# Kernel optimization log

Measured on AMD Instinct MI355X. Metric: run time of the kernel, lower is better.

## Reference

```python
import jax, jax.numpy as jnp
import numpy as np

B, SX, SY, D = 64, 512, 512, 1024


def setup_inputs() -> dict:
    key = jax.random.key(0)
    k1, k2, k3, k4 = jax.random.split(key, 4)
    x = jax.random.normal(k1, (B, SX, D), dtype=jnp.float32)
    y = jax.random.normal(k2, (B, SY, D), dtype=jnp.float32)
    # Keras 'uniform' init ~ U(-0.05, 0.05); scale kept small and realistic
    W = jax.random.uniform(k3, (D, D), dtype=jnp.float32, minval=-0.05, maxval=0.05)
    b = jax.random.uniform(k4, (D,), dtype=jnp.float32, minval=-0.05, maxval=0.05)
    return {"x": x, "y": y, "W": W, "b": b}


def reference(x, y, W, b):
    # proj: (x @ W + b) -> [B, Sx, D]
    proj = jnp.einsum('bsd,de->bse', x, W) + b
    # attention scores: proj @ y^T -> [B, Sx, Sy]
    att = jnp.einsum('bsd,btd->bst', proj, y)
    # row-wise stable softmax over last axis (matches manual max-subtract softmax)
    nor = jax.nn.softmax(att, axis=-1)
    # weighted sum over y -> [B, Sx, D]
    return jnp.einsum('bst,btd->bsd', nor, y)
```

## Files before the change

### kernel.cpp

```cpp
#include <hip/hip_runtime.h>


typedef float  f32x4  __attribute__((ext_vector_type(4)));
typedef _Float16 f16x8 __attribute__((ext_vector_type(8)));
typedef _Float16 f16x4 __attribute__((ext_vector_type(4)));
typedef __bf16 bf16x8 __attribute__((ext_vector_type(8)));
typedef __bf16 bf16x4 __attribute__((ext_vector_type(4)));

#define MFMA_F16(a, b, c)  __builtin_amdgcn_mfma_f32_16x16x32_f16((a), (b), (c), 0, 0, 0)
#define MFMA_BF16(a, b, c) __builtin_amdgcn_mfma_f32_16x16x32_bf16((a), (b), (c), 0, 0, 0)

__device__ __forceinline__ void async16(const void* g, void* lds) {
    __builtin_amdgcn_global_load_lds(
        (const __attribute__((address_space(1))) unsigned int*)g,
        (__attribute__((address_space(3))) unsigned int*)lds, 16, 0, 0);
}


__global__ void prep_y_kernel(const float* __restrict__ y, _Float16* __restrict__ yf,
                              _Float16* __restrict__ yT)
{
    __shared__ _Float16 LT[64][72];
    const int tid = threadIdx.x;
    const int b   = blockIdx.x >> 7;
    const int rem = blockIdx.x & 127;
    const int sy0 = (rem >> 4) * 64;
    const int d0  = (rem & 15) * 64;
    const int r0 = tid >> 4;
    const int c4 = (tid & 15) * 4;
    #pragma unroll
    for (int i = 0; i < 4; ++i) {
        const int r = r0 + i * 16;
        const float4 v = *(const float4*)&y[((size_t)b * 512 + sy0 + r) * 1024 + d0 + c4];
        const f16x4 hv = {(_Float16)v.x, (_Float16)v.y, (_Float16)v.z, (_Float16)v.w};
        *(f16x4*)&yf[((size_t)b * 512 + sy0 + r) * 1024 + d0 + c4] = hv;
        #pragma unroll
        for (int cc = 0; cc < 4; ++cc) {
            const int c = (cc + (tid & 3)) & 3;
            LT[c4 + c][r] = hv[c];
        }
    }
    __syncthreads();
    #pragma unroll
    for (int i = 0; i < 4; ++i) {
        const int dr = r0 + i * 16;
        const f16x4 v = *(const f16x4*)&LT[dr][(tid & 15) * 4];
        *(f16x4*)&yT[((size_t)b * 1024 + d0 + dr) * 512 + sy0 + (tid & 15) * 4] = v;
    }
}

__global__ void cvt_hl_kernel(const float4* __restrict__ in, f16x4* __restrict__ oh,
                              f16x4* __restrict__ ol, int n4)
{
    int i = blockIdx.x * blockDim.x + threadIdx.x;
    const int stride = gridDim.x * blockDim.x;
    for (; i < n4; i += stride) {
        const float4 v = in[i];
        const _Float16 h0 = (_Float16)v.x, h1 = (_Float16)v.y,
                       h2 = (_Float16)v.z, h3 = (_Float16)v.w;
        oh[i] = (f16x4){h0, h1, h2, h3};
        ol[i] = (f16x4){(_Float16)(v.x - (float)h0), (_Float16)(v.y - (float)h1),
                        (_Float16)(v.z - (float)h2), (_Float16)(v.w - (float)h3)};
    }
}

__global__ __launch_bounds__(256, 3)
void proj_f16_kernel(const _Float16* __restrict__ xh, const _Float16* __restrict__ xl,
                     const float* __restrict__ W, const float* __restrict__ bias,
                     char* __restrict__ outc)
{
    __shared__ _Float16 Xh[128][32];
    __shared__ _Float16 Xl[128][32];
    __shared__ _Float16 Wf[128][32];

    const int tid = threadIdx.x, lane = tid & 63, wave = tid >> 6;
    const int swz = (blockIdx.x & 7) * 256 + (blockIdx.x >> 3);
    const int m0 = (swz >> 3) * 128, n0 = (swz & 7) * 128;
    const int wm = (wave >> 1) * 64, wn = (wave & 1) * 64;
    const int ar = lane & 15;
    const int qs  = ((lane >> 4) ^ ((lane >> 1) & 3)) * 8;
    const int gcS = ((lane & 3) ^ ((lane >> 3) & 3)) * 8;

    f32x4 acc[4][4];
    #pragma unroll
    for (int i = 0; i < 4; ++i)
        #pragma unroll
        for (int j = 0; j < 4; ++j)
            acc[i][j] = (f32x4){0.f, 0.f, 0.f, 0.f};

    const int lrow = lane >> 2;
    const int wkb = tid & 7;
    const int wqn = tid >> 3;
    const int wn4 = wqn * 4;

    for (int k0 = 0; k0 < 1024; k0 += 32) {
        __syncthreads();
        #pragma unroll
        for (int t = 0; t < 2; ++t) {
            const int r = wave * 32 + t * 16 + lrow;
            async16(&xh[(size_t)(m0 + r) * 1024 + k0 + gcS], &Xh[wave * 32 + t * 16][0]);
            async16(&xl[(size_t)(m0 + r) * 1024 + k0 + gcS], &Xl[wave * 32 + t * 16][0]);
        }
        {
            const size_t wb = (size_t)(k0 + wkb * 4) * 1024 + n0 + wn4;
            const float4 v0 = *(const float4*)&W[wb];
            const float4 v1 = *(const float4*)&W[wb + 1024];
            const float4 v2 = *(const float4*)&W[wb + 2048];
            const float4 v3 = *(const float4*)&W[wb + 3072];
            const float rv[4][4] = {{v0.x, v0.y, v0.z, v0.w},
                                    {v1.x, v1.y, v1.z, v1.w},
                                    {v2.x, v2.y, v2.z, v2.w},
                                    {v3.x, v3.y, v3.z, v3.w}};
            #pragma unroll
            for (int j = 0; j < 4; ++j) {
                const int R = wn4 + j;
                const f16x4 hv = {(_Float16)rv[0][j], (_Float16)rv[1][j],
                                  (_Float16)rv[2][j], (_Float16)rv[3][j]};
                const int c = (wkb >> 1) ^ ((R >> 1) & 3);
                *(f16x4*)&Wf[R][c * 8 + (wkb & 1) * 4] = hv;
            }
        }
        __syncthreads();

        f16x8 ah[4], al[4], bf[4];
        #pragma unroll
        for (int f = 0; f < 4; ++f) {
            ah[f] = *(const f16x8*)&Xh[wm + f * 16 + ar][qs];
            al[f] = *(const f16x8*)&Xl[wm + f * 16 + ar][qs];
            bf[f] = *(const f16x8*)&Wf[wn + f * 16 + ar][qs];
        }
        #pragma unroll
        for (int i = 0; i < 4; ++i)
            #pragma unroll
            for (int j = 0; j < 4; ++j) {
                acc[i][j] = MFMA_F16(ah[i], bf[j], acc[i][j]);
                acc[i][j] = MFMA_F16(al[i], bf[j], acc[i][j]);
            }
    }

    const int q4 = (lane >> 4) * 4;
    #pragma unroll
    for (int j = 0; j < 4; ++j) {
        const int n = n0 + wn + j * 16 + ar;
        const float bv = bias[n];
        #pragma unroll
        for (int i = 0; i < 4; ++i)
            #pragma unroll
            for (int r = 0; r < 4; ++r) {
                const int R = m0 + wm + i * 16 + q4 + r;
                const float v = acc[i][j][r] + bv;
                const _Float16 h = (_Float16)v;
                const _Float16 l = (_Float16)(v - (float)h);
                _Float16* rowp = (_Float16*)(outc + (size_t)R * 4096);
                rowp[n] = h;
                rowp[1024 + n] = l;
            }
    }
}

__global__ __launch_bounds__(256, 2)
void attn_f16_kernel(const _Float16* __restrict__ yf, const _Float16* __restrict__ yT,
                     char* __restrict__ outc)
{
    __shared__ __align__(16) char smem[74752];
    _Float16 (*Yst)[32]   = (_Float16(*)[32])smem;
    _Float16 (*Pbuf)[520] = (_Float16(*)[520])smem;
    _Float16 (*Yt)[32]    = (_Float16(*)[32])(smem + 66560);

    const int tid = threadIdx.x, lane = tid & 63, wave = tid >> 6;
    const int swz = (blockIdx.x & 7) * 64 + (blockIdx.x >> 3);
    const int b = swz >> 3, sx0 = (swz & 7) * 64;
    const int pbase = b * 512 + sx0;
    const int ar = lane & 15, q = lane >> 4, qk = q * 8;
    const int qs  = (q ^ ((lane >> 1) & 3)) * 8;
    const int gcS = ((lane & 3) ^ ((lane >> 3) & 3)) * 8;
    const int lrow = lane >> 2;
    const size_t ybase = (size_t)b * 512 * 1024;

    f32x4 s[32];
    #pragma unroll
    for (int t = 0; t < 32; ++t) s[t] = (f32x4){0.f, 0.f, 0.f, 0.f};

    const _Float16* prow = (const _Float16*)(outc + (size_t)(pbase + wave * 16 + ar) * 4096);

    for (int k0 = 0; k0 < 1024; k0 += 32) {
        __syncthreads();
        #pragma unroll
        for (int t = 0; t < 8; ++t) {
            const int r = wave * 128 + t * 16 + lrow;
            async16(&yf[ybase + (size_t)r * 1024 + k0 + gcS], &Yst[wave * 128 + t * 16][0]);
        }
        const f16x8 a_h = *(const f16x8*)(prow + k0 + qk);
        const f16x8 a_l = *(const f16x8*)(prow + 1024 + k0 + qk);
        __syncthreads();
        #pragma unroll
        for (int t = 0; t < 32; ++t) {
            const f16x8 bfrag = *(const f16x8*)&Yst[t * 16 + ar][qs];
            s[t] = MFMA_F16(a_h, bfrag, s[t]);
            s[t] = MFMA_F16(a_l, bfrag, s[t]);
        }
    }

    #pragma unroll
    for (int r = 0; r < 4; ++r) {
        float m = -3.0e38f;
        #pragma unroll
        for (int t = 0; t < 32; ++t) m = fmaxf(m, s[t][r]);
        #pragma unroll
        for (int off = 1; off < 16; off <<= 1) m = fmaxf(m, __shfl_xor(m, off, 64));
        float sum = 0.f;
        #pragma unroll
        for (int t = 0; t < 32; ++t) {
            const float e = __expf(s[t][r] - m);
            s[t][r] = e;
            sum += e;
        }
        #pragma unroll
        for (int off = 1; off < 16; off <<= 1) sum += __shfl_xor(sum, off, 64);
        const float inv = 1.0f / sum;
        #pragma unroll
        for (int t = 0; t < 32; ++t) s[t][r] *= inv;
    }

    __syncthreads();
    #pragma unroll
    for (int t = 0; t < 32; ++t)
        #pragma unroll
        for (int r = 0; r < 4; ++r)
            Pbuf[wave * 16 + q * 4 + r][t * 16 + ar] = (_Float16)s[t][r];

    float* outF = (float*)outc;
    for (int dc = 0; dc < 8; ++dc) {
        f32x4 o[8];
        #pragma unroll
        for (int t = 0; t < 8; ++t) o[t] = (f32x4){0.f, 0.f, 0.f, 0.f};

        for (int k0 = 0; k0 < 512; k0 += 32) {
            __syncthreads();
            #pragma unroll
            for (int t = 0; t < 2; ++t) {
                const int r = wave * 32 + t * 16 + lrow;
                async16(&yT[(size_t)(b * 1024 + dc * 128 + r) * 512 + k0 + gcS],
                        &Yt[wave * 32 + t * 16][0]);
            }
            const f16x8 a = *(const f16x8*)&Pbuf[wave * 16 + ar][k0 + qk];
            __syncthreads();
            #pragma unroll
            for (int t = 0; t < 8; ++t) {
                const f16x8 bfrag = *(const f16x8*)&Yt[t * 16 + ar][qs];
                o[t] = MFMA_F16(a, bfrag, o[t]);
            }
        }
        #pragma unroll
        for (int t = 0; t < 8; ++t)
            #pragma unroll
            for (int r = 0; r < 4; ++r)
                outF[(size_t)(pbase + wave * 16 + q * 4 + r) * 1024 + dc * 128 + t * 16 + ar]
                    = o[t][r];
    }
}


__device__ __forceinline__ void cvt4(const float4 v, bf16x4& h, bf16x4& l) {
    const float f0 = v.x, f1 = v.y, f2 = v.z, f3 = v.w;
    const __bf16 h0 = (__bf16)f0, h1 = (__bf16)f1, h2 = (__bf16)f2, h3 = (__bf16)f3;
    h = (bf16x4){h0, h1, h2, h3};
    l = (bf16x4){(__bf16)(f0 - (float)h0), (__bf16)(f1 - (float)h1),
                 (__bf16)(f2 - (float)h2), (__bf16)(f3 - (float)h3)};
}

__global__ __launch_bounds__(256, 2)
void proj_kernel_fb(const float* __restrict__ x, const float* __restrict__ W,
                    const float* __restrict__ bias, float* __restrict__ proj)
{
    __shared__ __bf16 Ah[128][40];
    __shared__ __bf16 Al[128][40];
    __shared__ __bf16 Bh[128][40];
    __shared__ __bf16 Bl[128][40];

    const int tid = threadIdx.x, lane = tid & 63, wave = tid >> 6;
    const int wm = (wave >> 1) * 64, wn = (wave & 1) * 64;
    const int m0 = (blockIdx.x >> 3) * 128, n0 = (blockIdx.x & 7) * 128;
    const int ar = lane & 15, ak = (lane >> 4) * 8;

    f32x4 acc[4][4];
    #pragma unroll
    for (int i = 0; i < 4; ++i)
        #pragma unroll
        for (int j = 0; j < 4; ++j)
            acc[i][j] = (f32x4){0.f, 0.f, 0.f, 0.f};

    const int xr = tid >> 3, xc = (tid & 7) * 4;
    const int wkb = tid >> 5, wn4 = (tid & 31) * 4;

    for (int k0 = 0; k0 < 1024; k0 += 32) {
        __syncthreads();
        #pragma unroll
        for (int it = 0; it < 4; ++it) {
            const int r = xr + it * 32;
            const float4 v = *(const float4*)&x[(size_t)(m0 + r) * 1024 + k0 + xc];
            bf16x4 h, l; cvt4(v, h, l);
            *(bf16x4*)&Ah[r][xc] = h;
            *(bf16x4*)&Al[r][xc] = l;
        }
        {
            const size_t wb = (size_t)(k0 + wkb * 4) * 1024 + n0 + wn4;
            const float4 v0 = *(const float4*)&W[wb];
            const float4 v1 = *(const float4*)&W[wb + 1024];
            const float4 v2 = *(const float4*)&W[wb + 2048];
            const float4 v3 = *(const float4*)&W[wb + 3072];
            const float rv[4][4] = {{v0.x, v0.y, v0.z, v0.w},
                                    {v1.x, v1.y, v1.z, v1.w},
                                    {v2.x, v2.y, v2.z, v2.w},
                                    {v3.x, v3.y, v3.z, v3.w}};
            #pragma unroll
            for (int j = 0; j < 4; ++j) {
                bf16x4 h, l;
                #pragma unroll
                for (int kk = 0; kk < 4; ++kk) {
                    const float f = rv[kk][j];
                    const __bf16 hb = (__bf16)f;
                    h[kk] = hb;
                    l[kk] = (__bf16)(f - (float)hb);
                }
                *(bf16x4*)&Bh[wn4 + j][wkb * 4] = h;
                *(bf16x4*)&Bl[wn4 + j][wkb * 4] = l;
            }
        }
        __syncthreads();

        bf16x8 a_h[4], a_l[4], b_h[4], b_l[4];
        #pragma unroll
        for (int f = 0; f < 4; ++f) {
            a_h[f] = *(const bf16x8*)&Ah[wm + f * 16 + ar][ak];
            a_l[f] = *(const bf16x8*)&Al[wm + f * 16 + ar][ak];
            b_h[f] = *(const bf16x8*)&Bh[wn + f * 16 + ar][ak];
            b_l[f] = *(const bf16x8*)&Bl[wn + f * 16 + ar][ak];
        }
        #pragma unroll
        for (int i = 0; i < 4; ++i)
            #pragma unroll
            for (int j = 0; j < 4; ++j) {
                acc[i][j] = MFMA_BF16(a_h[i], b_h[j], acc[i][j]);
                acc[i][j] = MFMA_BF16(a_l[i], b_h[j], acc[i][j]);
                acc[i][j] = MFMA_BF16(a_h[i], b_l[j], acc[i][j]);
            }
    }

    const int q4 = (lane >> 4) * 4;
    #pragma unroll
    for (int j = 0; j < 4; ++j) {
        const int n = n0 + wn + j * 16 + ar;
        const float bv = bias[n];
        #pragma unroll
        for (int i = 0; i < 4; ++i) {
            const size_t base = (size_t)(m0 + wm + i * 16 + q4) * 1024 + n;
            #pragma unroll
            for (int r = 0; r < 4; ++r)
                proj[base + (size_t)r * 1024] = acc[i][j][r] + bv;
        }
    }
}

__global__ __launch_bounds__(256, 1)
void attn_kernel_fb(const float* __restrict__ y, float* __restrict__ out)
{
    __shared__ __bf16 Ph[64][40];
    __shared__ __bf16 Pl[64][40];
    __shared__ __bf16 Yh[128][40];
    __shared__ __bf16 Yl[128][40];
    __shared__ __bf16 Pbuf[64][520];

    const int tid = threadIdx.x, lane = tid & 63, wave = tid >> 6;
    const int b = blockIdx.x >> 3, sx0 = (blockIdx.x & 7) * 64;
    const size_t ybase = (size_t)b * 512 * 1024;
    const size_t pbase = ((size_t)b * 512 + sx0) * 1024;
    const int ar = lane & 15, ak = (lane >> 4) * 8, q = lane >> 4;

    f32x4 s[4][8];
    #pragma unroll
    for (int nb = 0; nb < 4; ++nb)
        #pragma unroll
        for (int f = 0; f < 8; ++f)
            s[nb][f] = (f32x4){0.f, 0.f, 0.f, 0.f};

    const int pr = tid >> 3, pc = (tid & 7) * 4;

    for (int k0 = 0; k0 < 1024; k0 += 32) {
        __syncthreads();
        #pragma unroll
        for (int it = 0; it < 2; ++it) {
            const int r = pr + it * 32;
            const float4 v = *(const float4*)&out[pbase + (size_t)r * 1024 + k0 + pc];
            bf16x4 h, l; cvt4(v, h, l);
            *(bf16x4*)&Ph[r][pc] = h;
            *(bf16x4*)&Pl[r][pc] = l;
        }
        #pragma unroll
        for (int nb = 0; nb < 4; ++nb) {
            if (nb) __syncthreads();
            const int sy0 = nb * 128;
            #pragma unroll
            for (int it = 0; it < 4; ++it) {
                const int r = pr + it * 32;
                const float4 v = *(const float4*)&y[ybase + (size_t)(sy0 + r) * 1024 + k0 + pc];
                bf16x4 h, l; cvt4(v, h, l);
                *(bf16x4*)&Yh[r][pc] = h;
                *(bf16x4*)&Yl[r][pc] = l;
            }
            __syncthreads();
            const bf16x8 a_h = *(const bf16x8*)&Ph[wave * 16 + ar][ak];
            const bf16x8 a_l = *(const bf16x8*)&Pl[wave * 16 + ar][ak];
            #pragma unroll
            for (int f = 0; f < 8; ++f) {
                const bf16x8 b_h = *(const bf16x8*)&Yh[f * 16 + ar][ak];
                const bf16x8 b_l = *(const bf16x8*)&Yl[f * 16 + ar][ak];
                s[nb][f] = MFMA_BF16(a_h, b_h, s[nb][f]);
                s[nb][f] = MFMA_BF16(a_l, b_h, s[nb][f]);
                s[nb][f] = MFMA_BF16(a_h, b_l, s[nb][f]);
            }
        }
    }

    #pragma unroll
    for (int r = 0; r < 4; ++r) {
        float m = -3.0e38f;
        #pragma unroll
        for (int nb = 0; nb < 4; ++nb)
            #pragma unroll
            for (int f = 0; f < 8; ++f)
                m = fmaxf(m, s[nb][f][r]);
        #pragma unroll
        for (int off = 1; off < 16; off <<= 1)
            m = fmaxf(m, __shfl_xor(m, off, 64));
        float sum = 0.f;
        #pragma unroll
        for (int nb = 0; nb < 4; ++nb)
            #pragma unroll
            for (int f = 0; f < 8; ++f) {
                const float e = __expf(s[nb][f][r] - m);
                s[nb][f][r] = e;
                sum += e;
            }
        #pragma unroll
        for (int off = 1; off < 16; off <<= 1)
            sum += __shfl_xor(sum, off, 64);
        const float inv = 1.0f / sum;
        #pragma unroll
        for (int nb = 0; nb < 4; ++nb)
            #pragma unroll
            for (int f = 0; f < 8; ++f)
                s[nb][f][r] *= inv;
    }
    #pragma unroll
    for (int nb = 0; nb < 4; ++nb)
        #pragma unroll
        for (int f = 0; f < 8; ++f)
            #pragma unroll
            for (int r = 0; r < 4; ++r)
                Pbuf[wave * 16 + q * 4 + r][nb * 128 + f * 16 + ar] = (__bf16)s[nb][f][r];

    const int y2kb = tid >> 5, y2n4 = (tid & 31) * 4;
    for (int d0 = 0; d0 < 1024; d0 += 128) {
        f32x4 o[8];
        #pragma unroll
        for (int f = 0; f < 8; ++f) o[f] = (f32x4){0.f, 0.f, 0.f, 0.f};

        for (int k0 = 0; k0 < 512; k0 += 32) {
            __syncthreads();
            const size_t yb = ybase + (size_t)(k0 + y2kb * 4) * 1024 + d0 + y2n4;
            const float4 v0 = *(const float4*)&y[yb];
            const float4 v1 = *(const float4*)&y[yb + 1024];
            const float4 v2 = *(const float4*)&y[yb + 2048];
            const float4 v3 = *(const float4*)&y[yb + 3072];
            const float rv[4][4] = {{v0.x, v0.y, v0.z, v0.w},
                                    {v1.x, v1.y, v1.z, v1.w},
                                    {v2.x, v2.y, v2.z, v2.w},
                                    {v3.x, v3.y, v3.z, v3.w}};
            #pragma unroll
            for (int j = 0; j < 4; ++j) {
                const bf16x4 h = (bf16x4){(__bf16)rv[0][j], (__bf16)rv[1][j],
                                          (__bf16)rv[2][j], (__bf16)rv[3][j]};
                *(bf16x4*)&Yh[y2n4 + j][y2kb * 4] = h;
            }
            __syncthreads();
            const bf16x8 a = *(const bf16x8*)&Pbuf[wave * 16 + ar][k0 + ak];
            #pragma unroll
            for (int f = 0; f < 8; ++f) {
                const bf16x8 bb = *(const bf16x8*)&Yh[f * 16 + ar][ak];
                o[f] = MFMA_BF16(a, bb, o[f]);
            }
        }
        #pragma unroll
        for (int f = 0; f < 8; ++f)
            #pragma unroll
            for (int r = 0; r < 4; ++r)
                out[pbase + (size_t)(wave * 16 + q * 4 + r) * 1024 + d0 + f * 16 + ar] = o[f][r];
    }
}


extern "C" void kernel_launch(void* const* d_in, const int* in_sizes, int n_in,
                              void* d_out, int out_size, void* d_ws, size_t ws_size,
                              hipStream_t stream) {
    (void)in_sizes; (void)n_in; (void)out_size;
    const float* x    = (const float*)d_in[0];
    const float* y    = (const float*)d_in[1];
    const float* W    = (const float*)d_in[2];
    const float* bias = (const float*)d_in[3];

    if (ws_size >= 268435456ULL) {
        _Float16* yf = (_Float16*)d_ws;
        _Float16* yT = yf + 33554432;
        _Float16* xh = yT + 33554432;
        _Float16* xl = xh + 33554432;
        prep_y_kernel<<<dim3(8192), dim3(256), 0, stream>>>(y, yf, yT);
        cvt_hl_kernel<<<dim3(2048), dim3(256), 0, stream>>>((const float4*)x, (f16x4*)xh,
                                                            (f16x4*)xl, 8388608);
        proj_f16_kernel<<<dim3(2048), dim3(256), 0, stream>>>(xh, xl, W, bias, (char*)d_out);
        attn_f16_kernel<<<dim3(512), dim3(256), 0, stream>>>(yf, yT, (char*)d_out);
    } else {
        float* out = (float*)d_out;
        proj_kernel_fb<<<dim3(256 * 8), dim3(256), 0, stream>>>(x, W, bias, out);
        attn_kernel_fb<<<dim3(64 * 8), dim3(256), 0, stream>>>(y, out);
    }
}
```

Before: 737.8 us.

## Pre-transpose W to fp16 and restructure attention kernel wave tiling with prefetch

Adds a prep kernel that converts W to a transposed fp16 copy so the projection kernel can stream it with async LDS loads instead of converting in-loop. The attention kernel is rewritten so each wave owns a slice of the key/feature dimension for all 64 query rows. This lets each LDS B fragment be reused across four A fragments. The row softmax then needs a cross-wave max and sum reduction through shared memory. The global-to-LDS loads are software-prefetched one step ahead using explicit waitcnt barriers. Costs include extra workspace, a small extra launch, and a prefetch scheme whose safety rests on the waitcnt ordering within each wave.

```diff
diff --git a/kernel.cpp b/kernel.cpp
--- a/kernel.cpp
+++ b/kernel.cpp
@@ -9,6 +9,11 @@
 
 #define MFMA_F16(a, b, c)  __builtin_amdgcn_mfma_f32_16x16x32_f16((a), (b), (c), 0, 0, 0)
 #define MFMA_BF16(a, b, c) __builtin_amdgcn_mfma_f32_16x16x32_bf16((a), (b), (c), 0, 0, 0)
+
+#define WAIT_VM0()  do { asm volatile("s_waitcnt vmcnt(0)" ::: "memory"); \
+                         __builtin_amdgcn_sched_barrier(0); } while (0)
+#define WAIT_LGKM0() do { asm volatile("s_waitcnt lgkmcnt(0)" ::: "memory"); \
+                          __builtin_amdgcn_sched_barrier(0); } while (0)
 
 __device__ __forceinline__ void async16(const void* g, void* lds) {
     __builtin_amdgcn_global_load_lds(
@@ -46,6 +51,34 @@
         const int dr = r0 + i * 16;
         const f16x4 v = *(const f16x4*)&LT[dr][(tid & 15) * 4];
         *(f16x4*)&yT[((size_t)b * 1024 + d0 + dr) * 512 + sy0 + (tid & 15) * 4] = v;
+    }
+}
+
+__global__ void prep_w_kernel(const float* __restrict__ W, _Float16* __restrict__ WT)
+{
+    __shared__ _Float16 LT[64][72];
+    const int tid = threadIdx.x;
+    const int k0 = (blockIdx.x >> 4) * 64;
+    const int n0 = (blockIdx.x & 15) * 64;
+    const int r0 = tid >> 4;
+    const int c4 = (tid & 15) * 4;
+    #pragma unroll
+    for (int i = 0; i < 4; ++i) {
+        const int r = r0 + i * 16;
+        const float4 v = *(const float4*)&W[(size_t)(k0 + r) * 1024 + n0 + c4];
+        const f16x4 hv = {(_Float16)v.x, (_Float16)v.y, (_Float16)v.z, (_Float16)v.w};
+        #pragma unroll
+        for (int cc = 0; cc < 4; ++cc) {
+            const int c = (cc + (tid & 3)) & 3;
+            LT[c4 + c][r] = hv[c];
+        }
+    }
+    __syncthreads();
+    #pragma unroll
+    for (int i = 0; i < 4; ++i) {
+        const int dr = r0 + i * 16;
+        const f16x4 v = *(const f16x4*)&LT[dr][(tid & 15) * 4];
+        *(f16x4*)&WT[(size_t)(n0 + dr) * 1024 + k0 + (tid & 15) * 4] = v;
     }
 }
 
@@ -64,10 +97,11 @@
     }
 }
 
+template <bool PRE>
 __global__ __launch_bounds__(256, 3)
 void proj_f16_kernel(const _Float16* __restrict__ xh, const _Float16* __restrict__ xl,
-                     const float* __restrict__ W, const float* __restrict__ bias,
-                     char* __restrict__ outc)
+                     const _Float16* __restrict__ WT, const float* __restrict__ W,
+                     const float* __restrict__ bias, char* __restrict__ outc)
 {
     __shared__ _Float16 Xh[128][32];
     __shared__ _Float16 Xl[128][32];
@@ -90,8 +124,7 @@
 
     const int lrow = lane >> 2;
     const int wkb = tid & 7;
-    const int wqn = tid >> 3;
-    const int wn4 = wqn * 4;
+    const int wn4 = (tid >> 3) * 4;
 
     for (int k0 = 0; k0 < 1024; k0 += 32) {
         __syncthreads();
@@ -100,8 +133,10 @@
             const int r = wave * 32 + t * 16 + lrow;
             async16(&xh[(size_t)(m0 + r) * 1024 + k0 + gcS], &Xh[wave * 32 + t * 16][0]);
             async16(&xl[(size_t)(m0 + r) * 1024 + k0 + gcS], &Xl[wave * 32 + t * 16][0]);
-        }
-        {
+            if constexpr (PRE)
+                async16(&WT[(size_t)(n0 + r) * 1024 + k0 + gcS], &Wf[wave * 32 + t * 16][0]);
+        }
+        if constexpr (!PRE) {
             const size_t wb = (size_t)(k0 + wkb * 4) * 1024 + n0 + wn4;
             const float4 v0 = *(const float4*)&W[wb];
             const float4 v1 = *(const float4*)&W[wb + 1024];
@@ -162,10 +197,11 @@
 void attn_f16_kernel(const _Float16* __restrict__ yf, const _Float16* __restrict__ yT,
                      char* __restrict__ outc)
 {
-    __shared__ __align__(16) char smem[74752];
+    __shared__ __align__(16) char smem[76800];
     _Float16 (*Yst)[32]   = (_Float16(*)[32])smem;
     _Float16 (*Pbuf)[520] = (_Float16(*)[520])smem;
     _Float16 (*Yt)[32]    = (_Float16(*)[32])(smem + 66560);
+    float*    Red         = (float*)(smem + 74752);
 
     const int tid = threadIdx.x, lane = tid & 63, wave = tid >> 6;
     const int swz = (blockIdx.x & 7) * 64 + (blockIdx.x >> 3);
@@ -177,86 +213,191 @@
     const int lrow = lane >> 2;
     const size_t ybase = (size_t)b * 512 * 1024;
 
-    f32x4 s[32];
-    #pragma unroll
-    for (int t = 0; t < 32; ++t) s[t] = (f32x4){0.f, 0.f, 0.f, 0.f};
-
-    const _Float16* prow = (const _Float16*)(outc + (size_t)(pbase + wave * 16 + ar) * 4096);
-
-    for (int k0 = 0; k0 < 1024; k0 += 32) {
-        __syncthreads();
-        #pragma unroll
-        for (int t = 0; t < 8; ++t) {
-            const int r = wave * 128 + t * 16 + lrow;
-            async16(&yf[ybase + (size_t)r * 1024 + k0 + gcS], &Yst[wave * 128 + t * 16][0]);
-        }
-        const f16x8 a_h = *(const f16x8*)(prow + k0 + qk);
-        const f16x8 a_l = *(const f16x8*)(prow + 1024 + k0 + qk);
-        __syncthreads();
-        #pragma unroll
-        for (int t = 0; t < 32; ++t) {
-            const f16x8 bfrag = *(const f16x8*)&Yst[t * 16 + ar][qs];
-            s[t] = MFMA_F16(a_h, bfrag, s[t]);
-            s[t] = MFMA_F16(a_l, bfrag, s[t]);
-        }
-    }
-
-    #pragma unroll
-    for (int r = 0; r < 4; ++r) {
-        float m = -3.0e38f;
-        #pragma unroll
-        for (int t = 0; t < 32; ++t) m = fmaxf(m, s[t][r]);
-        #pragma unroll
-        for (int off = 1; off < 16; off <<= 1) m = fmaxf(m, __shfl_xor(m, off, 64));
-        float sum = 0.f;
-        #pragma unroll
-        for (int t = 0; t < 32; ++t) {
-            const float e = __expf(s[t][r] - m);
-            s[t][r] = e;
-            sum += e;
-        }
-        #pragma unroll
-        for (int off = 1; off < 16; off <<= 1) sum += __shfl_xor(sum, off, 64);
-        const float inv = 1.0f / sum;
-        #pragma unroll
-        for (int t = 0; t < 32; ++t) s[t][r] *= inv;
-    }
-
+    f32x4 s2[4][8];
+    #pragma unroll
+    for (int ri = 0; ri < 4; ++ri)
+        #pragma unroll
+        for (int t = 0; t < 8; ++t)
+            s2[ri][t] = (f32x4){0.f, 0.f, 0.f, 0.f};
+
+    const char* aptr = outc + (size_t)(pbase + ar) * 4096;
+
+    #pragma unroll
+    for (int t = 0; t < 8; ++t) {
+        const int r = wave * 128 + t * 16 + lrow;
+        async16(&yf[ybase + (size_t)r * 1024 + gcS], &Yst[wave * 128 + t * 16][0]);
+    }
+    f16x8 aH[4], aL[4];
+    #pragma unroll
+    for (int ri = 0; ri < 4; ++ri) {
+        aH[ri] = *(const f16x8*)(aptr + (size_t)ri * 65536 + (size_t)qk * 2);
+        aL[ri] = *(const f16x8*)(aptr + (size_t)ri * 65536 + 2048 + (size_t)qk * 2);
+    }
+
+    for (int kk = 0; kk < 32; ++kk) {
+        WAIT_VM0();
+        f16x8 bf0[8];
+        #pragma unroll
+        for (int t = 0; t < 8; ++t)
+            bf0[t] = *(const f16x8*)&Yst[wave * 128 + t * 16 + ar][qs];
+        WAIT_LGKM0();
+        if (kk < 31) {
+            const int k1 = (kk + 1) * 32;
+            #pragma unroll
+            for (int t = 0; t < 8; ++t) {
+                const int r = wave * 128 + t * 16 + lrow;
+                async16(&yf[ybase + (size_t)r * 1024 + k1 + gcS],
+                        &Yst[wave * 128 + t * 16][0]);
+            }
+        }
+        #pragma unroll
+        for (int ri = 0; ri < 4; ++ri)
+            #pragma unroll
+            for (int t = 0; t < 8; ++t) {
+                s2[ri][t] = MFMA_F16(aH[ri], bf0[t], s2[ri][t]);
+                s2[ri][t] = MFMA_F16(aL[ri], bf0[t], s2[ri][t]);
+            }
+        if (kk < 31) {
+            const int k1 = (kk + 1) * 32;
+            #pragma unroll
+            for (int ri = 0; ri < 4; ++ri) {
+                aH[ri] = *(const f16x8*)(aptr + (size_t)ri * 65536 + (size_t)(k1 + qk) * 2);
+                aL[ri] = *(const f16x8*)(aptr + (size_t)ri * 65536 + 2048
+                                         + (size_t)(k1 + qk) * 2);
+            }
+        }
+    }
+
+    float pm[4][4];
+    #pragma unroll
+    for (int ri = 0; ri < 4; ++ri)
+        #pragma unroll
+        for (int r = 0; r < 4; ++r) {
+            float m = -3.0e38f;
+            #pragma unroll
+            for (int t = 0; t < 8; ++t) m = fmaxf(m, s2[ri][t][r]);
+            pm[ri][r] = m;
+        }
+    #pragma unroll
+    for (int off = 1; off < 16; off <<= 1)
+        #pragma unroll
+        for (int ri = 0; ri < 4; ++ri)
+            #pragma unroll
+            for (int r = 0; r < 4; ++r)
+                pm[ri][r] = fmaxf(pm[ri][r], __shfl_xor(pm[ri][r], off, 64));
+    if (ar == 0) {
+        #pragma unroll
+        for (int ri = 0; ri < 4; ++ri)
+            #pragma unroll
+            for (int r = 0; r < 4; ++r)
+                Red[wave * 64 + ri * 16 + q * 4 + r] = pm[ri][r];
+    }
     __syncthreads();
-    #pragma unroll
-    for (int t = 0; t < 32; ++t)
-        #pragma unroll
-        for (int r = 0; r < 4; ++r)
-            Pbuf[wave * 16 + q * 4 + r][t * 16 + ar] = (_Float16)s[t][r];
+    float gm[4][4];
+    #pragma unroll
+    for (int ri = 0; ri < 4; ++ri)
+        #pragma unroll
+        for (int r = 0; r < 4; ++r) {
+            const int row = ri * 16 + q * 4 + r;
+            gm[ri][r] = fmaxf(fmaxf(Red[row], Red[64 + row]),
+                              fmaxf(Red[128 + row], Red[192 + row]));
+        }
+    float ps[4][4];
+    #pragma unroll
+    for (int ri = 0; ri < 4; ++ri)
+        #pragma unroll
+        for (int r = 0; r < 4; ++r) {
+            float sum = 0.f;
+            #pragma unroll
+            for (int t = 0; t < 8; ++t) {
+                const float e = __expf(s2[ri][t][r] - gm[ri][r]);
+                s2[ri][t][r] = e;
+                sum += e;
+            }
+            ps[ri][r] = sum;
+        }
+    #pragma unroll
+    for (int off = 1; off < 16; off <<= 1)
+        #pragma unroll
+        for (int ri = 0; ri < 4; ++ri)
+            #pragma unroll
+            for (int r = 0; r < 4; ++r)
+                ps[ri][r] += __shfl_xor(ps[ri][r], off, 64);
+    if (ar == 0) {
+        #pragma unroll
+        for (int ri = 0; ri < 4; ++ri)
+            #pragma unroll
+            for (int r = 0; r < 4; ++r)
+                Red[256 + wave * 64 + ri * 16 + q * 4 + r] = ps[ri][r];
+    }
+    __syncthreads();
+    float inv[4][4];
+    #pragma unroll
+    for (int ri = 0; ri < 4; ++ri)
+        #pragma unroll
+        for (int r = 0; r < 4; ++r) {
+            const int row = 256 + ri * 16 + q * 4 + r;
+            inv[ri][r] = 1.0f / (Red[row] + Red[64 + row] + Red[128 + row] + Red[192 + row]);
+        }
+    #pragma unroll
+    for (int ri = 0; ri < 4; ++ri)
+        #pragma unroll
+        for (int t = 0; t < 8; ++t)
+            #pragma unroll
+            for (int r = 0; r < 4; ++r)
+                Pbuf[ri * 16 + q * 4 + r][wave * 128 + t * 16 + ar]
+                    = (_Float16)(s2[ri][t][r] * inv[ri][r]);
+    __syncthreads();
 
     float* outF = (float*)outc;
     for (int dc = 0; dc < 8; ++dc) {
-        f32x4 o[8];
-        #pragma unroll
-        for (int t = 0; t < 8; ++t) o[t] = (f32x4){0.f, 0.f, 0.f, 0.f};
-
-        for (int k0 = 0; k0 < 512; k0 += 32) {
-            __syncthreads();
-            #pragma unroll
-            for (int t = 0; t < 2; ++t) {
-                const int r = wave * 32 + t * 16 + lrow;
-                async16(&yT[(size_t)(b * 1024 + dc * 128 + r) * 512 + k0 + gcS],
-                        &Yt[wave * 32 + t * 16][0]);
-            }
-            const f16x8 a = *(const f16x8*)&Pbuf[wave * 16 + ar][k0 + qk];
-            __syncthreads();
-            #pragma unroll
-            for (int t = 0; t < 8; ++t) {
-                const f16x8 bfrag = *(const f16x8*)&Yt[t * 16 + ar][qs];
-                o[t] = MFMA_F16(a, bfrag, o[t]);
-            }
-        }
-        #pragma unroll
-        for (int t = 0; t < 8; ++t)
-            #pragma unroll
-            for (int r = 0; r < 4; ++r)
-                outF[(size_t)(pbase + wave * 16 + q * 4 + r) * 1024 + dc * 128 + t * 16 + ar]
-                    = o[t][r];
+        f32x4 o2[4][2];
+        #pragma unroll
+        for (int ri = 0; ri < 4; ++ri)
+            #pragma unroll
+            for (int t = 0; t < 2; ++t)
+                o2[ri][t] = (f32x4){0.f, 0.f, 0.f, 0.f};
+
+        WAIT_LGKM0();
+        #pragma unroll
+        for (int t = 0; t < 2; ++t) {
+            const int r = wave * 32 + t * 16 + lrow;
+            async16(&yT[(size_t)(b * 1024 + dc * 128 + r) * 512 + gcS],
+                    &Yt[wave * 32 + t * 16][0]);
+        }
+        for (int kk = 0; kk < 16; ++kk) {
+            WAIT_VM0();
+            f16x8 a2[4], b2[2];
+            #pragma unroll
+            for (int ri = 0; ri < 4; ++ri)
+                a2[ri] = *(const f16x8*)&Pbuf[ri * 16 + ar][kk * 32 + qk];
+            #pragma unroll
+            for (int t = 0; t < 2; ++t)
+                b2[t] = *(const f16x8*)&Yt[wave * 32 + t * 16 + ar][qs];
+            WAIT_LGKM0();
+            if (kk < 15) {
+                const int k1 = (kk + 1) * 32;
+                #pragma unroll
+                for (int t = 0; t < 2; ++t) {
+                    const int r = wave * 32 + t * 16 + lrow;
+                    async16(&yT[(size_t)(b * 1024 + dc * 128 + r) * 512 + k1 + gcS],
+                            &Yt[wave * 32 + t * 16][0]);
+                }
+            }
+            #pragma unroll
+            for (int ri = 0; ri < 4; ++ri)
+                #pragma unroll
+                for (int t = 0; t < 2; ++t)
+                    o2[ri][t] = MFMA_F16(a2[ri], b2[t], o2[ri][t]);
+        }
+        #pragma unroll
+        for (int ri = 0; ri < 4; ++ri)
+            #pragma unroll
+            for (int t = 0; t < 2; ++t)
+                #pragma unroll
+                for (int r = 0; r < 4; ++r)
+                    outF[(size_t)(pbase + ri * 16 + q * 4 + r) * 1024
+                         + dc * 128 + wave * 32 + t * 16 + ar] = o2[ri][t][r];
     }
 }
 
@@ -514,10 +655,20 @@
         _Float16* yT = yf + 33554432;
         _Float16* xh = yT + 33554432;
         _Float16* xl = xh + 33554432;
+        _Float16* WT = xl + 33554432;
+        const bool pre = ws_size >= 268435456ULL + 2097152ULL;
+
         prep_y_kernel<<<dim3(8192), dim3(256), 0, stream>>>(y, yf, yT);
         cvt_hl_kernel<<<dim3(2048), dim3(256), 0, stream>>>((const float4*)x, (f16x4*)xh,
                                                             (f16x4*)xl, 8388608);
-        proj_f16_kernel<<<dim3(2048), dim3(256), 0, stream>>>(xh, xl, W, bias, (char*)d_out);
+        if (pre) {
+            prep_w_kernel<<<dim3(256), dim3(256), 0, stream>>>(W, WT);
+            proj_f16_kernel<true><<<dim3(2048), dim3(256), 0, stream>>>(xh, xl, WT, W, bias,
+                                                                        (char*)d_out);
+        } else {
+            proj_f16_kernel<false><<<dim3(2048), dim3(256), 0, stream>>>(xh, xl, nullptr, W,
+                                                                         bias, (char*)d_out);
+        }
         attn_f16_kernel<<<dim3(512), dim3(256), 0, stream>>>(yf, yT, (char*)d_out);
     } else {
         float* out = (float*)d_out;
```

Result: faster. 703.4 us (-4.7%).
